# Optimization experiments

Measured on AMD Instinct MI355X. Metric: run time of the kernel, lower is better.

## Reference

```python
import jax, jax.numpy as jnp
import numpy as np

NEG_SLOPE = 0.2  # PyG GATConv default


def setup_inputs() -> dict:
    key = jax.random.key(0)
    k1, k2, k3, k4, k5, k6 = jax.random.split(key, 6)
    N, F_in, F_out, E = 50000, 512, 256, 400000
    x = jax.random.normal(k1, (N, F_in), dtype=jnp.float32)
    adj = jax.random.randint(k2, (2, E), 0, N, dtype=jnp.int64)  # [2, E] edge_index (src, dst)
    glorot = lambda k, shape: jax.random.uniform(
        k, shape, jnp.float32, -1.0, 1.0) * np.sqrt(6.0 / (shape[0] + shape[-1]))
    W = glorot(k3, (F_in, F_out))
    att_src = glorot(k4, (F_out,))
    att_dst = glorot(k5, (F_out,))
    bias = jnp.zeros((F_out,), dtype=jnp.float32)
    return {"x": x, "adj": adj, "W": W, "att_src": att_src, "att_dst": att_dst, "bias": bias}


def reference(x, adj, W, att_src, att_dst, bias):
    N = x.shape[0]
    # add self loops (PyG GATConv default add_self_loops=True)
    loops = jnp.arange(N, dtype=adj.dtype)
    src = jnp.concatenate([adj[0], loops])
    dst = jnp.concatenate([adj[1], loops])

    h = x @ W                          # [N, F_out] projected features
    a_src = h @ att_src                # [N] per-node source attention term
    a_dst = h @ att_dst                # [N]
    e = a_src[src] + a_dst[dst]        # [E+N] edge logits
    e = jnp.where(e > 0, e, NEG_SLOPE * e)  # leaky_relu

    # per-destination softmax over incoming edges (numerically stable)
    m = jax.ops.segment_max(e, dst, num_segments=N)
    ex = jnp.exp(e - m[dst])
    denom = jax.ops.segment_sum(ex, dst, num_segments=N)
    alpha = ex / denom[dst]            # [E+N]

    # weighted scatter-aggregate of source messages
    out = jax.ops.segment_sum(alpha[:, None] * h[src], dst, num_segments=N)
    out = out + bias
    return jax.nn.relu(out)
```

## Files before the change

kernel.cpp:

```cpp
#include <hip/hip_runtime.h>
#include <hip/hip_bf16.h>

typedef __attribute__((ext_vector_type(8))) short bf16x8;
typedef __attribute__((ext_vector_type(4))) float f32x4;
typedef unsigned short u16;

#define F_IN 512
#define F_OUT 256
#define NEG_SLOPE 0.2f

__device__ __forceinline__ float leaky(float e) { return e > 0.f ? e : NEG_SLOPE * e; }

__device__ __forceinline__ u16 f2bf(float x) {
    __hip_bfloat16 h = __float2bfloat16(x);
    return *reinterpret_cast<u16*>(&h);
}
__device__ __forceinline__ void bf2x2(unsigned p, float& a, float& b) {
    a = __uint_as_float(p << 16);
    b = __uint_as_float(p & 0xffff0000u);
}

__device__ __forceinline__ void dma16(const void* g, void* l) {
    __builtin_amdgcn_global_load_lds((const __attribute__((address_space(1))) void*)g,
                                     (__attribute__((address_space(3))) void*)l, 16, 0, 0);
}

__global__ void k_transpose(const float* __restrict__ W, u16* __restrict__ Wt) {
    int t = blockIdx.x * 256 + threadIdx.x;
    int k = t >> 8;
    int n = t & 255;
    Wt[n * F_IN + k] = f2bf(W[k * F_OUT + n]);
}

__global__ __launch_bounds__(256) void k_gemm(const float* __restrict__ X,
                                              const u16* __restrict__ Wt,
                                              u16* __restrict__ Hb, int N) {
    __shared__ float sA[128 * 32];
    __shared__ u16 sB[128 * 32];
    const int tid = threadIdx.x;
    const int wave = tid >> 6, lane = tid & 63;
    const int wm = (wave >> 1) * 64, wn = (wave & 1) * 64;
    const int tile_m = blockIdx.y * 128, tile_n = blockIdx.x * 128;

    f32x4 acc[4][4];
#pragma unroll
    for (int i = 0; i < 4; i++)
#pragma unroll
        for (int j = 0; j < 4; j++) acc[i][j] = (f32x4){0.f, 0.f, 0.f, 0.f};

    const int a_row_in = lane >> 3;
    const int a_gc = (lane & 7) ^ a_row_in;
    const int b_row_in = lane >> 2;
    const int b_gc = (lane & 3) ^ ((lane >> 3) & 3);

    for (int kb = 0; kb < F_IN / 32; ++kb) {
#pragma unroll
        for (int t = 0; t < 4; ++t) {
            int r0 = wave * 32 + t * 8;
            int grow = tile_m + r0 + a_row_in;
            if (grow >= N) grow = N - 1;
            dma16(&X[(size_t)grow * F_IN + kb * 32 + a_gc * 4], &sA[r0 * 32]);
        }
#pragma unroll
        for (int t = 0; t < 2; ++t) {
            int r0 = wave * 32 + t * 16;
            int grow = tile_n + r0 + b_row_in;
            dma16(&Wt[(size_t)grow * F_IN + kb * 32 + b_gc * 8], &sB[r0 * 32]);
        }
        __syncthreads();

        const int lm = lane & 15, q = lane >> 4;
        bf16x8 af[4], bfr[4];
#pragma unroll
        for (int i = 0; i < 4; i++) {
            const int arow = wm + i * 16 + lm;
            const int s7 = arow & 7;
            const float4 c0 = *(const float4*)&sA[arow * 32 + (((2 * q) ^ s7) << 2)];
            const float4 c1 = *(const float4*)&sA[arow * 32 + (((2 * q + 1) ^ s7) << 2)];
            u16 a8[8] = {f2bf(c0.x), f2bf(c0.y), f2bf(c0.z), f2bf(c0.w),
                         f2bf(c1.x), f2bf(c1.y), f2bf(c1.z), f2bf(c1.w)};
            af[i] = *(const bf16x8*)a8;
            const int brow = wn + i * 16 + lm;
            bfr[i] = *(const bf16x8*)&sB[brow * 32 + ((q ^ ((lm >> 1) & 3)) << 3)];
        }
#pragma unroll
        for (int i = 0; i < 4; i++)
#pragma unroll
            for (int j = 0; j < 4; j++)
                acc[i][j] = __builtin_amdgcn_mfma_f32_16x16x32_bf16(af[i], bfr[j], acc[i][j], 0, 0, 0);
        __syncthreads();
    }

    const int lc = lane & 15, lr4 = (lane >> 4) * 4;
    for (int i = 0; i < 4; i++)
        for (int j = 0; j < 4; j++) {
#pragma unroll
            for (int r = 0; r < 4; r++) {
                int row = tile_m + wm + i * 16 + lr4 + r;
                int col = tile_n + wn + j * 16 + lc;
                if (row < N) Hb[(size_t)row * F_OUT + col] = f2bf(acc[i][j][r]);
            }
        }
}

__global__ __launch_bounds__(256) void k_dots(const u16* __restrict__ Hb,
                                              const float* __restrict__ att_src,
                                              const float* __restrict__ att_dst,
                                              float* __restrict__ aS, float* __restrict__ aD,
                                              int* __restrict__ deg, int N) {
    int wave = threadIdx.x >> 6, lane = threadIdx.x & 63;
    int row = blockIdx.x * 4 + wave;
    if (row >= N) return;
    uint2 rv = *(const uint2*)&Hb[(size_t)row * F_OUT + lane * 4];
    float h0, h1, h2, h3;
    bf2x2(rv.x, h0, h1);
    bf2x2(rv.y, h2, h3);
    const float4 as = *(const float4*)&att_src[lane * 4];
    const float4 ad = *(const float4*)&att_dst[lane * 4];
    float s1 = h0 * as.x + h1 * as.y + h2 * as.z + h3 * as.w;
    float s2 = h0 * ad.x + h1 * ad.y + h2 * ad.z + h3 * ad.w;
    for (int off = 32; off; off >>= 1) {
        s1 += __shfl_down(s1, off);
        s2 += __shfl_down(s2, off);
    }
    if (lane == 0) {
        aS[row] = s1;
        aD[row] = s2;
        deg[row] = 0;
    }
}

__global__ void k_deg(const int* __restrict__ dsts, int* __restrict__ deg, int E) {
    int e = blockIdx.x * 256 + threadIdx.x;
    if (e >= E) return;
    atomicAdd(&deg[dsts[e]], 1);
}

__global__ __launch_bounds__(256) void k_scan1(const int* __restrict__ deg,
                                               int* __restrict__ bsum, int N) {
    __shared__ int ws[4];
    int t = threadIdx.x;
    int i = blockIdx.x * 256 + t;
    int v = (i < N) ? deg[i] : 0;
    for (int off = 32; off; off >>= 1) v += __shfl_down(v, off);
    if ((t & 63) == 0) ws[t >> 6] = v;
    __syncthreads();
    if (t == 0) bsum[blockIdx.x] = ws[0] + ws[1] + ws[2] + ws[3];
}

__global__ __launch_bounds__(256) void k_scan2(const int* __restrict__ bsum,
                                               int* __restrict__ boff, int* __restrict__ offs,
                                               int nb, int N) {
    __shared__ int ss[256];
    int t = threadIdx.x;
    int v = (t < nb) ? bsum[t] : 0;
    ss[t] = v;
    __syncthreads();
    for (int off = 1; off < 256; off <<= 1) {
        int u = (t >= off) ? ss[t - off] : 0;
        __syncthreads();
        ss[t] += u;
        __syncthreads();
    }
    boff[t] = ss[t] - v;
    if (t == 255) offs[N] = ss[255];
}

__global__ __launch_bounds__(256) void k_scan3(const int* __restrict__ deg,
                                               const int* __restrict__ boff,
                                               int* __restrict__ offs, int* __restrict__ cur,
                                               int N) {
    __shared__ int ss[256];
    int t = threadIdx.x;
    int i = blockIdx.x * 256 + t;
    int v = (i < N) ? deg[i] : 0;
    ss[t] = v;
    __syncthreads();
    for (int off = 1; off < 256; off <<= 1) {
        int u = (t >= off) ? ss[t - off] : 0;
        __syncthreads();
        ss[t] += u;
        __syncthreads();
    }
    int ex = ss[t] - v + boff[blockIdx.x];
    if (i < N) {
        offs[i] = ex;
        cur[i] = ex;
    }
}

__global__ void k_edge_scatter(const int* __restrict__ srcs, const int* __restrict__ dsts,
                               const float* __restrict__ aS, const float* __restrict__ aD,
                               int* __restrict__ cur, int* __restrict__ csrS,
                               float* __restrict__ csrW, int E) {
    int e = blockIdx.x * 256 + threadIdx.x;
    if (e >= E) return;
    int s = srcs[e], d = dsts[e];
    float ex = __expf(leaky(aS[s] + aD[d]));
    int pos = atomicAdd(&cur[d], 1);
    csrS[pos] = s;
    csrW[pos] = ex;
}

__global__ __launch_bounds__(256) void k_aggregate(const u16* __restrict__ Hb,
                                                   const float* __restrict__ aS,
                                                   const float* __restrict__ aD,
                                                   const int* __restrict__ offs,
                                                   const int* __restrict__ csrS,
                                                   const float* __restrict__ csrW,
                                                   const float* __restrict__ bias,
                                                   float* __restrict__ out, int N) {
    int wave = threadIdx.x >> 6, lane = threadIdx.x & 63;
    int i = blockIdx.x * 4 + wave;
    if (i >= N) return;
    float sex = __expf(leaky(aS[i] + aD[i]));

    uint2 rv = *(const uint2*)&Hb[(size_t)i * F_OUT + lane * 4];
    float f0, f1, f2, f3;
    bf2x2(rv.x, f0, f1);
    bf2x2(rv.y, f2, f3);
    float4 acc = {sex * f0, sex * f1, sex * f2, sex * f3};
    float wsum = sex;

    int beg = offs[i], end = offs[i + 1];
    int k = beg;
    for (; k + 4 <= end; k += 4) {
        int s0 = csrS[k], s1 = csrS[k + 1], s2 = csrS[k + 2], s3 = csrS[k + 3];
        float w0 = csrW[k], w1 = csrW[k + 1], w2 = csrW[k + 2], w3 = csrW[k + 3];
        uint2 g0 = *(const uint2*)&Hb[(size_t)s0 * F_OUT + lane * 4];
        uint2 g1 = *(const uint2*)&Hb[(size_t)s1 * F_OUT + lane * 4];
        uint2 g2 = *(const uint2*)&Hb[(size_t)s2 * F_OUT + lane * 4];
        uint2 g3 = *(const uint2*)&Hb[(size_t)s3 * F_OUT + lane * 4];
        wsum += w0 + w1 + w2 + w3;
        bf2x2(g0.x, f0, f1); bf2x2(g0.y, f2, f3);
        acc.x += w0 * f0; acc.y += w0 * f1; acc.z += w0 * f2; acc.w += w0 * f3;
        bf2x2(g1.x, f0, f1); bf2x2(g1.y, f2, f3);
        acc.x += w1 * f0; acc.y += w1 * f1; acc.z += w1 * f2; acc.w += w1 * f3;
        bf2x2(g2.x, f0, f1); bf2x2(g2.y, f2, f3);
        acc.x += w2 * f0; acc.y += w2 * f1; acc.z += w2 * f2; acc.w += w2 * f3;
        bf2x2(g3.x, f0, f1); bf2x2(g3.y, f2, f3);
        acc.x += w3 * f0; acc.y += w3 * f1; acc.z += w3 * f2; acc.w += w3 * f3;
    }
    for (; k < end; ++k) {
        int s = csrS[k];
        float w = csrW[k];
        uint2 r = *(const uint2*)&Hb[(size_t)s * F_OUT + lane * 4];
        wsum += w;
        bf2x2(r.x, f0, f1);
        bf2x2(r.y, f2, f3);
        acc.x += w * f0;
        acc.y += w * f1;
        acc.z += w * f2;
        acc.w += w * f3;
    }
    float inv = 1.f / wsum;
    const float4 bv = *(const float4*)&bias[lane * 4];
    float4 o;
    o.x = acc.x * inv + bv.x;
    o.y = acc.y * inv + bv.y;
    o.z = acc.z * inv + bv.z;
    o.w = acc.w * inv + bv.w;
    o.x = o.x > 0.f ? o.x : 0.f;
    o.y = o.y > 0.f ? o.y : 0.f;
    o.z = o.z > 0.f ? o.z : 0.f;
    o.w = o.w > 0.f ? o.w : 0.f;
    *(float4*)&out[(size_t)i * F_OUT + lane * 4] = o;
}

extern "C" void kernel_launch(void* const* d_in, const int* in_sizes, int n_in,
                              void* d_out, int out_size, void* d_ws, size_t ws_size,
                              hipStream_t stream) {
    const float* X = (const float*)d_in[0];
    const int* adj = (const int*)d_in[1];
    const float* W = (const float*)d_in[2];
    const float* att_src = (const float*)d_in[3];
    const float* att_dst = (const float*)d_in[4];
    const float* bias = (const float*)d_in[5];
    float* out = (float*)d_out;

    const int N = in_sizes[0] / F_IN;
    const int E = in_sizes[1] / 2;
    const int* srcs = adj;
    const int* dsts = adj + E;
    const int nb = (N + 255) / 256;

    char* p = (char*)d_ws;
    auto take = [&](size_t b) -> char* {
        char* q = p;
        p += (b + 255) & ~(size_t)255;
        return q;
    };
    u16* Hb = (u16*)take((size_t)N * F_OUT * sizeof(u16));
    u16* Wt = (u16*)take((size_t)F_IN * F_OUT * sizeof(u16));
    float* aS = (float*)take((size_t)N * sizeof(float));
    float* aD = (float*)take((size_t)N * sizeof(float));
    int* deg = (int*)take((size_t)N * sizeof(int));
    int* offs = (int*)take((size_t)(N + 1) * sizeof(int));
    int* cur = (int*)take((size_t)N * sizeof(int));
    int* bsum = (int*)take((size_t)256 * sizeof(int));
    int* boff = (int*)take((size_t)256 * sizeof(int));
    int* csrS = (int*)take((size_t)E * sizeof(int));
    float* csrW = (float*)take((size_t)E * sizeof(float));

    k_transpose<<<(F_IN * F_OUT) / 256, 256, 0, stream>>>(W, Wt);
    dim3 ggrid((F_OUT + 127) / 128, (N + 127) / 128);
    k_gemm<<<ggrid, 256, 0, stream>>>(X, Wt, Hb, N);
    k_dots<<<(N + 3) / 4, 256, 0, stream>>>(Hb, att_src, att_dst, aS, aD, deg, N);
    k_deg<<<(E + 255) / 256, 256, 0, stream>>>(dsts, deg, E);
    k_scan1<<<nb, 256, 0, stream>>>(deg, bsum, N);
    k_scan2<<<1, 256, 0, stream>>>(bsum, boff, offs, nb, N);
    k_scan3<<<nb, 256, 0, stream>>>(deg, boff, offs, cur, N);
    k_edge_scatter<<<(E + 255) / 256, 256, 0, stream>>>(srcs, dsts, aS, aD, cur, csrS, csrW, E);
    k_aggregate<<<(N + 3) / 4, 256, 0, stream>>>(Hb, aS, aD, offs, csrS, csrW, bias, out, N);
}
```

Before: 290.8 us.

## Register-prefetch X in GEMM with bf16 LDS staging; unroll aggregation loop by eight

The GEMM no longer uses direct global-to-LDS DMA of fp32 X. It now prefetches the next 64-wide K slice of X into registers while MFMAs run on the current slice. X is converted to bf16 once before the swizzled LDS store, the K step doubles to 64, and launch bounds request 3 blocks per CU. The gather-aggregate kernel also unrolls its edge loop to 8 to keep more neighbor loads in flight. The cost is extra register pressure from the prefetch buffers and a software-pipelined structure that may limit occupancy.

```diff
diff --git a/kernel.cpp b/kernel.cpp
--- a/kernel.cpp
+++ b/kernel.cpp
@@ -18,11 +18,6 @@
 __device__ __forceinline__ void bf2x2(unsigned p, float& a, float& b) {
     a = __uint_as_float(p << 16);
     b = __uint_as_float(p & 0xffff0000u);
-}
-
-__device__ __forceinline__ void dma16(const void* g, void* l) {
-    __builtin_amdgcn_global_load_lds((const __attribute__((address_space(1))) void*)g,
-                                     (__attribute__((address_space(3))) void*)l, 16, 0, 0);
 }
 
 __global__ void k_transpose(const float* __restrict__ W, u16* __restrict__ Wt) {
@@ -32,11 +27,11 @@
     Wt[n * F_IN + k] = f2bf(W[k * F_OUT + n]);
 }
 
-__global__ __launch_bounds__(256) void k_gemm(const float* __restrict__ X,
-                                              const u16* __restrict__ Wt,
-                                              u16* __restrict__ Hb, int N) {
-    __shared__ float sA[128 * 32];
-    __shared__ u16 sB[128 * 32];
+__global__ __launch_bounds__(256, 3) void k_gemm(const float* __restrict__ X,
+                                                 const u16* __restrict__ Wt,
+                                                 u16* __restrict__ Hb, int N) {
+    __shared__ u16 sA[128 * 64];
+    __shared__ u16 sB[128 * 64];
     const int tid = threadIdx.x;
     const int wave = tid >> 6, lane = tid & 63;
     const int wm = (wave >> 1) * 64, wn = (wave & 1) * 64;
@@ -48,48 +43,72 @@
 #pragma unroll
         for (int j = 0; j < 4; j++) acc[i][j] = (f32x4){0.f, 0.f, 0.f, 0.f};
 
-    const int a_row_in = lane >> 3;
-    const int a_gc = (lane & 7) ^ a_row_in;
-    const int b_row_in = lane >> 2;
-    const int b_gc = (lane & 3) ^ ((lane >> 3) & 3);
-
-    for (int kb = 0; kb < F_IN / 32; ++kb) {
-#pragma unroll
-        for (int t = 0; t < 4; ++t) {
-            int r0 = wave * 32 + t * 8;
-            int grow = tile_m + r0 + a_row_in;
-            if (grow >= N) grow = N - 1;
-            dma16(&X[(size_t)grow * F_IN + kb * 32 + a_gc * 4], &sA[r0 * 32]);
+    const int r0 = tid >> 2;
+    const int p0 = tid & 3;
+
+    float4 px[2][2][2];
+
+#define ISSUE_X(KB)                                                                       \
+    do {                                                                                  \
+        _Pragma("unroll") for (int j = 0; j < 2; ++j) {                                   \
+            int arow = tile_m + r0 + j * 64;                                              \
+            if (arow >= N) arow = N - 1;    \
+            _Pragma("unroll") for (int h = 0; h < 2; ++h) {                               \
+                const float4* xa =                                                        \
+                    (const float4*)&X[(size_t)arow * F_IN + (KB)*64 + h * 32 + p0 * 8];   \
+                px[j][h][0] = xa[0];                                                      \
+                px[j][h][1] = xa[1];                                                      \
+            }                                                                             \
+        }                                                                                 \
+    } while (0)
+
+    ISSUE_X(0);
+
+    for (int kb = 0; kb < F_IN / 64; ++kb) {
+        bf16x8 vb[2][2];
+#pragma unroll
+        for (int j = 0; j < 2; ++j)
+#pragma unroll
+            for (int h = 0; h < 2; ++h)
+                vb[j][h] = *(const bf16x8*)&Wt[(size_t)(tile_n + r0 + j * 64) * F_IN +
+                                               kb * 64 + h * 32 + p0 * 8];
+#pragma unroll
+        for (int j = 0; j < 2; ++j) {
+            const int row = r0 + j * 64;
+#pragma unroll
+            for (int h = 0; h < 2; ++h) {
+                const int ch = (h * 4 + p0) ^ (row & 7);
+                u16 a8[8] = {f2bf(px[j][h][0].x), f2bf(px[j][h][0].y), f2bf(px[j][h][0].z),
+                             f2bf(px[j][h][0].w), f2bf(px[j][h][1].x), f2bf(px[j][h][1].y),
+                             f2bf(px[j][h][1].z), f2bf(px[j][h][1].w)};
+                *(bf16x8*)&sA[row * 64 + ch * 8] = *(const bf16x8*)a8;
+                *(bf16x8*)&sB[row * 64 + ch * 8] = vb[j][h];
+            }
         }
-#pragma unroll
-        for (int t = 0; t < 2; ++t) {
-            int r0 = wave * 32 + t * 16;
-            int grow = tile_n + r0 + b_row_in;
-            dma16(&Wt[(size_t)grow * F_IN + kb * 32 + b_gc * 8], &sB[r0 * 32]);
+        __syncthreads();
+
+        if (kb + 1 < F_IN / 64) ISSUE_X(kb + 1);
+
+        const int lm = lane & 15, q = lane >> 4;
+#pragma unroll
+        for (int s = 0; s < 2; ++s) {
+            bf16x8 af[4], bfr[4];
+#pragma unroll
+            for (int i = 0; i < 4; i++) {
+                const int ch = (s * 4 + q) ^ (lm & 7);
+                af[i] = *(const bf16x8*)&sA[(wm + i * 16 + lm) * 64 + ch * 8];
+                bfr[i] = *(const bf16x8*)&sB[(wn + i * 16 + lm) * 64 + ch * 8];
+            }
+#pragma unroll
+            for (int i = 0; i < 4; i++)
+#pragma unroll
+                for (int j = 0; j < 4; j++)
+                    acc[i][j] =
+                        __builtin_amdgcn_mfma_f32_16x16x32_bf16(af[i], bfr[j], acc[i][j], 0, 0, 0);
         }
         __syncthreads();
-
-        const int lm = lane & 15, q = lane >> 4;
-        bf16x8 af[4], bfr[4];
-#pragma unroll
-        for (int i = 0; i < 4; i++) {
-            const int arow = wm + i * 16 + lm;
-            const int s7 = arow & 7;
-            const float4 c0 = *(const float4*)&sA[arow * 32 + (((2 * q) ^ s7) << 2)];
-            const float4 c1 = *(const float4*)&sA[arow * 32 + (((2 * q + 1) ^ s7) << 2)];
-            u16 a8[8] = {f2bf(c0.x), f2bf(c0.y), f2bf(c0.z), f2bf(c0.w),
-                         f2bf(c1.x), f2bf(c1.y), f2bf(c1.z), f2bf(c1.w)};
-            af[i] = *(const bf16x8*)a8;
-            const int brow = wn + i * 16 + lm;
-            bfr[i] = *(const bf16x8*)&sB[brow * 32 + ((q ^ ((lm >> 1) & 3)) << 3)];
-        }
-#pragma unroll
-        for (int i = 0; i < 4; i++)
-#pragma unroll
-            for (int j = 0; j < 4; j++)
-                acc[i][j] = __builtin_amdgcn_mfma_f32_16x16x32_bf16(af[i], bfr[j], acc[i][j], 0, 0, 0);
-        __syncthreads();
-    }
+    }
+#undef ISSUE_X
 
     const int lc = lane & 15, lr4 = (lane >> 4) * 4;
     for (int i = 0; i < 4; i++)
@@ -224,35 +243,31 @@
 
     int beg = offs[i], end = offs[i + 1];
     int k = beg;
+
+#define EDGE_STEP(IDX)                                                     \
+    do {                                                                   \
+        float w_ = csrW[IDX];                                              \
+        uint2 g_ = *(const uint2*)&Hb[(size_t)csrS[IDX] * F_OUT + lane * 4]; \
+        wsum += w_;                                                        \
+        float a_, b_, c_, d_;                                              \
+        bf2x2(g_.x, a_, b_);                                               \
+        bf2x2(g_.y, c_, d_);                                               \
+        acc.x += w_ * a_;                                                  \
+        acc.y += w_ * b_;                                                  \
+        acc.z += w_ * c_;                                                  \
+        acc.w += w_ * d_;                                                  \
+    } while (0)
+
+    for (; k + 8 <= end; k += 8) {
+        EDGE_STEP(k); EDGE_STEP(k + 1); EDGE_STEP(k + 2); EDGE_STEP(k + 3);
+        EDGE_STEP(k + 4); EDGE_STEP(k + 5); EDGE_STEP(k + 6); EDGE_STEP(k + 7);
+    }
     for (; k + 4 <= end; k += 4) {
-        int s0 = csrS[k], s1 = csrS[k + 1], s2 = csrS[k + 2], s3 = csrS[k + 3];
-        float w0 = csrW[k], w1 = csrW[k + 1], w2 = csrW[k + 2], w3 = csrW[k + 3];
-        uint2 g0 = *(const uint2*)&Hb[(size_t)s0 * F_OUT + lane * 4];
-        uint2 g1 = *(const uint2*)&Hb[(size_t)s1 * F_OUT + lane * 4];
-        uint2 g2 = *(const uint2*)&Hb[(size_t)s2 * F_OUT + lane * 4];
-        uint2 g3 = *(const uint2*)&Hb[(size_t)s3 * F_OUT + lane * 4];
-        wsum += w0 + w1 + w2 + w3;
-        bf2x2(g0.x, f0, f1); bf2x2(g0.y, f2, f3);
-        acc.x += w0 * f0; acc.y += w0 * f1; acc.z += w0 * f2; acc.w += w0 * f3;
-        bf2x2(g1.x, f0, f1); bf2x2(g1.y, f2, f3);
-        acc.x += w1 * f0; acc.y += w1 * f1; acc.z += w1 * f2; acc.w += w1 * f3;
-        bf2x2(g2.x, f0, f1); bf2x2(g2.y, f2, f3);
-        acc.x += w2 * f0; acc.y += w2 * f1; acc.z += w2 * f2; acc.w += w2 * f3;
-        bf2x2(g3.x, f0, f1); bf2x2(g3.y, f2, f3);
-        acc.x += w3 * f0; acc.y += w3 * f1; acc.z += w3 * f2; acc.w += w3 * f3;
-    }
-    for (; k < end; ++k) {
-        int s = csrS[k];
-        float w = csrW[k];
-        uint2 r = *(const uint2*)&Hb[(size_t)s * F_OUT + lane * 4];
-        wsum += w;
-        bf2x2(r.x, f0, f1);
-        bf2x2(r.y, f2, f3);
-        acc.x += w * f0;
-        acc.y += w * f1;
-        acc.z += w * f2;
-        acc.w += w * f3;
-    }
+        EDGE_STEP(k); EDGE_STEP(k + 1); EDGE_STEP(k + 2); EDGE_STEP(k + 3);
+    }
+    for (; k < end; ++k) EDGE_STEP(k);
+#undef EDGE_STEP
+
     float inv = 1.f / wsum;
     const float4 bv = *(const float4*)&bias[lane * 4];
     float4 o;
```

Result: slower. 300.8 us (+3.5%).

## Register-prefetch GEMM tiles, convert X to bf16 before LDS, shrink M tile

Applied to the files above, without the earlier changes.

Replaces the direct global-to-LDS DMA loads in the projection GEMM with register prefetching of the next K block, issued while the current block is computed. X is converted to bf16 once before being stored to LDS, and a padded row stride replaces the XOR swizzle. The M tile drops from 128 to 64 rows, doubling the grid and reducing accumulators per wave, which trades per-block reuse for more occupancy and overlap. Only the GEMM stage changes; the graph stages are untouched.

```diff
diff --git a/kernel.cpp b/kernel.cpp
--- a/kernel.cpp
+++ b/kernel.cpp
@@ -8,6 +8,7 @@
 #define F_IN 512
 #define F_OUT 256
 #define NEG_SLOPE 0.2f
+#define LSTRIDE 40
 
 __device__ __forceinline__ float leaky(float e) { return e > 0.f ? e : NEG_SLOPE * e; }
 
@@ -18,11 +19,6 @@
 __device__ __forceinline__ void bf2x2(unsigned p, float& a, float& b) {
     a = __uint_as_float(p << 16);
     b = __uint_as_float(p & 0xffff0000u);
-}
-
-__device__ __forceinline__ void dma16(const void* g, void* l) {
-    __builtin_amdgcn_global_load_lds((const __attribute__((address_space(1))) void*)g,
-                                     (__attribute__((address_space(3))) void*)l, 16, 0, 0);
 }
 
 __global__ void k_transpose(const float* __restrict__ W, u16* __restrict__ Wt) {
@@ -35,64 +31,67 @@
 __global__ __launch_bounds__(256) void k_gemm(const float* __restrict__ X,
                                               const u16* __restrict__ Wt,
                                               u16* __restrict__ Hb, int N) {
-    __shared__ float sA[128 * 32];
-    __shared__ u16 sB[128 * 32];
+    __shared__ short sA[64 * LSTRIDE];
+    __shared__ short sB[128 * LSTRIDE];
     const int tid = threadIdx.x;
     const int wave = tid >> 6, lane = tid & 63;
-    const int wm = (wave >> 1) * 64, wn = (wave & 1) * 64;
-    const int tile_m = blockIdx.y * 128, tile_n = blockIdx.x * 128;
-
-    f32x4 acc[4][4];
-#pragma unroll
-    for (int i = 0; i < 4; i++)
+    const int wm = (wave >> 1) * 32, wn = (wave & 1) * 64;
+    const int tile_m = blockIdx.y * 64, tile_n = blockIdx.x * 128;
+
+    f32x4 acc[2][4];
+#pragma unroll
+    for (int i = 0; i < 2; i++)
 #pragma unroll
         for (int j = 0; j < 4; j++) acc[i][j] = (f32x4){0.f, 0.f, 0.f, 0.f};
 
-    const int a_row_in = lane >> 3;
-    const int a_gc = (lane & 7) ^ a_row_in;
-    const int b_row_in = lane >> 2;
-    const int b_gc = (lane & 3) ^ ((lane >> 3) & 3);
+    const int r0 = tid >> 2;
+    const int p0 = tid & 3;
+
+    float4 px[2];
+    bf16x8 pw[2];
+
+#define ISSUE_LOADS(KB)                                                                  \
+    do {                                                                                 \
+        int arow = tile_m + r0;                                                          \
+        if (arow >= N) arow = N - 1;       \
+        const float4* xa = (const float4*)&X[(size_t)arow * F_IN + (KB)*32 + p0 * 8];    \
+        px[0] = xa[0];                                                                   \
+        px[1] = xa[1];                                                                   \
+        _Pragma("unroll") for (int j = 0; j < 2; ++j) {                                  \
+            pw[j] = *(const bf16x8*)&Wt[(size_t)(tile_n + r0 + j * 64) * F_IN +          \
+                                        (KB)*32 + p0 * 8];                               \
+        }                                                                                \
+    } while (0)
+
+    ISSUE_LOADS(0);
 
     for (int kb = 0; kb < F_IN / 32; ++kb) {
-#pragma unroll
-        for (int t = 0; t < 4; ++t) {
-            int r0 = wave * 32 + t * 8;
-            int grow = tile_m + r0 + a_row_in;
-            if (grow >= N) grow = N - 1;
-            dma16(&X[(size_t)grow * F_IN + kb * 32 + a_gc * 4], &sA[r0 * 32]);
-        }
-#pragma unroll
-        for (int t = 0; t < 2; ++t) {
-            int r0 = wave * 32 + t * 16;
-            int grow = tile_n + r0 + b_row_in;
-            dma16(&Wt[(size_t)grow * F_IN + kb * 32 + b_gc * 8], &sB[r0 * 32]);
-        }
-        __syncthreads();
-
-        const int lm = lane & 15, q = lane >> 4;
-        bf16x8 af[4], bfr[4];
-#pragma unroll
-        for (int i = 0; i < 4; i++) {
-            const int arow = wm + i * 16 + lm;
-            const int s7 = arow & 7;
-            const float4 c0 = *(const float4*)&sA[arow * 32 + (((2 * q) ^ s7) << 2)];
-            const float4 c1 = *(const float4*)&sA[arow * 32 + (((2 * q + 1) ^ s7) << 2)];
-            u16 a8[8] = {f2bf(c0.x), f2bf(c0.y), f2bf(c0.z), f2bf(c0.w),
-                         f2bf(c1.x), f2bf(c1.y), f2bf(c1.z), f2bf(c1.w)};
-            af[i] = *(const bf16x8*)a8;
-            const int brow = wn + i * 16 + lm;
-            bfr[i] = *(const bf16x8*)&sB[brow * 32 + ((q ^ ((lm >> 1) & 3)) << 3)];
-        }
-#pragma unroll
-        for (int i = 0; i < 4; i++)
+        u16 a8[8] = {f2bf(px[0].x), f2bf(px[0].y), f2bf(px[0].z), f2bf(px[0].w),
+                     f2bf(px[1].x), f2bf(px[1].y), f2bf(px[1].z), f2bf(px[1].w)};
+        *(bf16x8*)&sA[r0 * LSTRIDE + p0 * 8] = *(const bf16x8*)a8;
+        *(bf16x8*)&sB[r0 * LSTRIDE + p0 * 8] = pw[0];
+        *(bf16x8*)&sB[(r0 + 64) * LSTRIDE + p0 * 8] = pw[1];
+        __syncthreads();
+
+        if (kb + 1 < F_IN / 32) ISSUE_LOADS(kb + 1);
+
+        const int lm = lane & 15, lk = (lane >> 4) * 8;
+        bf16x8 af[2], bfr[4];
+#pragma unroll
+        for (int i = 0; i < 2; i++) af[i] = *(const bf16x8*)&sA[(wm + i * 16 + lm) * LSTRIDE + lk];
+#pragma unroll
+        for (int j = 0; j < 4; j++) bfr[j] = *(const bf16x8*)&sB[(wn + j * 16 + lm) * LSTRIDE + lk];
+#pragma unroll
+        for (int i = 0; i < 2; i++)
 #pragma unroll
             for (int j = 0; j < 4; j++)
                 acc[i][j] = __builtin_amdgcn_mfma_f32_16x16x32_bf16(af[i], bfr[j], acc[i][j], 0, 0, 0);
         __syncthreads();
     }
+#undef ISSUE_LOADS
 
     const int lc = lane & 15, lr4 = (lane >> 4) * 4;
-    for (int i = 0; i < 4; i++)
+    for (int i = 0; i < 2; i++)
         for (int j = 0; j < 4; j++) {
 #pragma unroll
             for (int r = 0; r < 4; r++) {
@@ -303,7 +302,7 @@
     float* csrW = (float*)take((size_t)E * sizeof(float));
 
     k_transpose<<<(F_IN * F_OUT) / 256, 256, 0, stream>>>(W, Wt);
-    dim3 ggrid((F_OUT + 127) / 128, (N + 127) / 128);
+    dim3 ggrid((F_OUT + 127) / 128, (N + 63) / 64);
     k_gemm<<<ggrid, 256, 0, stream>>>(X, Wt, Hb, N);
     k_dots<<<(N + 3) / 4, 256, 0, stream>>>(Hb, att_src, att_dst, aS, aD, deg, N);
     k_deg<<<(E + 255) / 256, 256, 0, stream>>>(dsts, deg, E);
```

Result: no change. 293.2 us (+0.8%).
